# Kernel optimization log

Hardware: AMD Instinct MI355X
Metric: run time of the kernel (lower is better)

The kernel has to match this reference:

```python
import jax, jax.numpy as jnp
import numpy as np

N_NODES = 50000


def gcn_conv(x, src, dst, W, b, n):
    # PyG GCNConv: h = x @ W; add self-loops; sym-norm aggregate; + bias
    h = x @ W
    loop = jnp.arange(n, dtype=src.dtype)
    s = jnp.concatenate([src, loop])
    d = jnp.concatenate([dst, loop])
    deg = jax.ops.segment_sum(jnp.ones(s.shape[0], h.dtype), d, num_segments=n)
    dinv = jnp.where(deg > 0, jax.lax.rsqrt(deg), 0.0)
    norm = dinv[s] * dinv[d]  # [E+n]
    msg = h[s] * norm[:, None]  # [E+n, C] gather
    out = jax.ops.segment_sum(msg, d, num_segments=n)  # scatter-add
    return out + b


def mlp_decode(z, src, dst, Wa, ba, Wb, bb):
    feat = jnp.concatenate([z[src], z[dst]], axis=1)  # [P, 2*out]
    hid = jax.nn.relu(feat @ Wa + ba)
    return hid @ Wb + bb  # [P, 1]


def setup_inputs() -> dict:
    key = jax.random.key(0)
    ks = jax.random.split(key, 12)
    in_c, hid_c, out_c = 128, 128, 64
    E, P = 800000, 200000
    x = jax.random.normal(ks[0], (N_NODES, in_c), dtype=jnp.float32)
    edge_index = jax.random.randint(ks[1], (2, E), 0, N_NODES, dtype=jnp.int64)
    pos_edge_index = jax.random.randint(ks[2], (2, P), 0, N_NODES, dtype=jnp.int64)
    neg_edge_index = jax.random.randint(ks[3], (2, P), 0, N_NODES, dtype=jnp.int64)
    s1 = 1.0 / np.sqrt(in_c)
    s2 = 1.0 / np.sqrt(hid_c)
    s3 = 1.0 / np.sqrt(2 * out_c)
    W1 = jax.random.uniform(ks[4], (in_c, hid_c), jnp.float32, -s1, s1)
    b1 = jnp.zeros((hid_c,), jnp.float32)
    W2 = jax.random.uniform(ks[5], (hid_c, out_c), jnp.float32, -s2, s2)
    b2 = jnp.zeros((out_c,), jnp.float32)
    Wa = jax.random.uniform(ks[6], (2 * out_c, hid_c), jnp.float32, -s3, s3)
    ba = jax.random.uniform(ks[7], (hid_c,), jnp.float32, -s3, s3)
    Wb = jax.random.uniform(ks[8], (hid_c, 1), jnp.float32, -s2, s2)
    bb = jax.random.uniform(ks[9], (1,), jnp.float32, -s2, s2)
    return {"x": x, "edge_index": edge_index, "pos_edge_index": pos_edge_index,
            "neg_edge_index": neg_edge_index, "W1": W1, "b1": b1, "W2": W2,
            "b2": b2, "Wa": Wa, "ba": ba, "Wb": Wb, "bb": bb}


def reference(x, edge_index, pos_edge_index, neg_edge_index,
              W1, b1, W2, b2, Wa, ba, Wb, bb):
    src, dst = edge_index[0], edge_index[1]
    n = x.shape[0]
    z = gcn_conv(x, src, dst, W1, b1, n)
    z = jax.nn.relu(z)  # dropout disabled in eval mode
    z = gcn_conv(z, src, dst, W2, b2, n)
    pos_pred = mlp_decode(z, pos_edge_index[0], pos_edge_index[1], Wa, ba, Wb, bb)
    neg_pred = mlp_decode(z, neg_edge_index[0], neg_edge_index[1], Wa, ba, Wb, bb)
    return (pos_pred, neg_pred)
```

## Files before the change

### kernel.cpp

```cpp
#include <hip/hip_runtime.h>
#include <hip/hip_bf16.h>
#include <hip/hip_fp16.h>

#define NODES 50000
#define NEDGE 800000
#define NPRED 200000

typedef __attribute__((ext_vector_type(8))) short bf16x8;
typedef __attribute__((ext_vector_type(8))) unsigned short u16x8;
typedef __attribute__((ext_vector_type(4))) float f32x4;

__device__ inline float bf2f(unsigned short u) {
    union { unsigned int i; float f; } v; v.i = ((unsigned int)u) << 16; return v.f;
}
__device__ inline unsigned short f2bf(float f) {
    __hip_bfloat16 b = __float2bfloat16(f);
    return *(unsigned short*)&b;
}

__global__ __launch_bounds__(256) void rank_count4(const int* __restrict__ dstv, int* __restrict__ cnt,
                                                   int* __restrict__ rank, int E4) {
    int i = blockIdx.x * 256 + threadIdx.x;
    if (i < E4) {
        int4 d4 = ((const int4*)dstv)[i];
        int4 r4;
        r4.x = atomicAdd(&cnt[d4.x], 1);
        r4.y = atomicAdd(&cnt[d4.y], 1);
        r4.z = atomicAdd(&cnt[d4.z], 1);
        r4.w = atomicAdd(&cnt[d4.w], 1);
        ((int4*)rank)[i] = r4;
    }
}

__global__ __launch_bounds__(256) void scan_bsum(const int* __restrict__ cnt, int* __restrict__ bsum, int n) {
    __shared__ int s[256];
    int t = threadIdx.x, b = blockIdx.x;
    int base = b * 1024 + t * 4;
    int sum = 0;
#pragma unroll
    for (int j = 0; j < 4; ++j) { int i = base + j; if (i < n) sum += cnt[i]; }
    s[t] = sum; __syncthreads();
    for (int off = 128; off >= 1; off >>= 1) {
        if (t < off) s[t] += s[t + off];
        __syncthreads();
    }
    if (t == 0) bsum[b] = s[0];
}

__global__ void scan_boff(const int* __restrict__ bsum, int* __restrict__ boff, int nb,
                          int* __restrict__ row_ptr, int n) {
    int t = threadIdx.x;
    int v = (t < nb) ? bsum[t] : 0;
    int orig = v;
    for (int off = 1; off < 64; off <<= 1) {
        int u = __shfl_up(v, off, 64);
        if (t >= off) v += u;
    }
    boff[t] = v - orig;
    if (t == 63) row_ptr[n] = v;
}

__global__ __launch_bounds__(256) void scan_write(const int* __restrict__ cnt, const int* __restrict__ boff,
                                                  int* __restrict__ row_ptr, float* __restrict__ dinv, int n) {
    __shared__ int s[256];
    int t = threadIdx.x, b = blockIdx.x;
    int base = b * 1024 + t * 4;
    int v[4]; int sum = 0;
#pragma unroll
    for (int j = 0; j < 4; ++j) { int i = base + j; v[j] = (i < n) ? cnt[i] : 0; sum += v[j]; }
    s[t] = sum; __syncthreads();
    for (int off = 1; off < 256; off <<= 1) {
        int u = (t >= off) ? s[t - off] : 0;
        __syncthreads();
        s[t] += u;
        __syncthreads();
    }
    int run = s[t] - sum + boff[b];
#pragma unroll
    for (int j = 0; j < 4; ++j) {
        int i = base + j;
        if (i < n) {
            row_ptr[i] = run; run += v[j];
            dinv[i] = rsqrtf((float)(v[j] + 1));
        }
    }
}

__global__ __launch_bounds__(256) void csr_fill2(const int* __restrict__ ei, const int* __restrict__ rank,
                                                 const int* __restrict__ row_ptr, int* __restrict__ colv, int E4) {
    int i = blockIdx.x * 256 + threadIdx.x;
    if (i < E4) {
        int4 s4 = ((const int4*)ei)[i];
        int4 d4 = ((const int4*)(ei + NEDGE))[i];
        int4 r4 = ((const int4*)rank)[i];
        colv[row_ptr[d4.x] + r4.x] = s4.x;
        colv[row_ptr[d4.y] + r4.y] = s4.y;
        colv[row_ptr[d4.z] + r4.z] = s4.z;
        colv[row_ptr[d4.w] + r4.w] = s4.w;
    }
}

__global__ __launch_bounds__(256) void perm_all(const float* __restrict__ W1, const float* __restrict__ W2,
                                                const float* __restrict__ Wa,
                                                unsigned short* __restrict__ pW1,
                                                unsigned short* __restrict__ pW2,
                                                unsigned short* __restrict__ pWa) {
    int t = blockIdx.x * 256 + threadIdx.x;
    if (t >= 5120) return;
    const float* W; unsigned short* P; int N;
    if (t < 2048)      { W = W1; P = pW1; N = 128; }
    else if (t < 3072) { W = W2; P = pW2; N = 64;  t -= 2048; }
    else               { W = Wa; P = pWa; N = 128; t -= 3072; }
    int lane = t & 63;
    int kt = (t >> 6) & 3;
    int nt = t >> 8;
    int n = nt * 16 + (lane & 15);
    int k0 = kt * 32 + (lane >> 4) * 8;
#pragma unroll
    for (int j = 0; j < 8; ++j) P[t * 8 + j] = f2bf(W[(k0 + j) * N + n]);
}

template <int NT, bool AFP32>
__global__ __launch_bounds__(256) void gemm_mfma(const void* __restrict__ Xv,
                                                 const unsigned short* __restrict__ perm,
                                                 unsigned short* __restrict__ H, int M) {
    int w = blockIdx.x * 4 + (threadIdx.x >> 6);
    int m0 = w * 16;
    if (m0 >= M) return;
    int lane = threadIdx.x & 63;
    int m = lane & 15, q = lane >> 4;
    size_t row = (size_t)(m0 + m);
    bf16x8 a[4];
    if (AFP32) {
        const float* X = (const float*)Xv;
#pragma unroll
        for (int kt = 0; kt < 4; ++kt) {
            float4 f0 = *(const float4*)&X[row * 128 + kt * 32 + q * 8];
            float4 f1 = *(const float4*)&X[row * 128 + kt * 32 + q * 8 + 4];
            bf16x8 av;
            av[0] = (short)f2bf(f0.x); av[1] = (short)f2bf(f0.y);
            av[2] = (short)f2bf(f0.z); av[3] = (short)f2bf(f0.w);
            av[4] = (short)f2bf(f1.x); av[5] = (short)f2bf(f1.y);
            av[6] = (short)f2bf(f1.z); av[7] = (short)f2bf(f1.w);
            a[kt] = av;
        }
    } else {
        const unsigned short* X = (const unsigned short*)Xv;
#pragma unroll
        for (int kt = 0; kt < 4; ++kt)
            a[kt] = *(const bf16x8*)&X[row * 128 + kt * 32 + q * 8];
    }
    const int N = NT * 16;
#pragma unroll
    for (int nt = 0; nt < NT; ++nt) {
        f32x4 c = {0.f, 0.f, 0.f, 0.f};
#pragma unroll
        for (int kt = 0; kt < 4; ++kt) {
            bf16x8 b = *(const bf16x8*)(perm + (size_t)((nt * 4 + kt) * 64 + lane) * 8);
            c = __builtin_amdgcn_mfma_f32_16x16x32_bf16(a[kt], b, c, 0, 0, 0);
        }
#pragma unroll
        for (int r = 0; r < 4; ++r)
            H[(size_t)(m0 + q * 4 + r) * N + nt * 16 + m] = f2bf(c[r]);
    }
}

template <int C, bool RELU>
__global__ __launch_bounds__(256) void agg_bf16(const unsigned short* __restrict__ h,
                                                const int* __restrict__ row_ptr, const int* __restrict__ colv,
                                                const float* __restrict__ dinv, const float* __restrict__ bias,
                                                unsigned short* __restrict__ out) {
    constexpr int TPN = C / 8;
    constexpr int NPB = 256 / TPN;
    int d = blockIdx.x * NPB + threadIdx.x / TPN;
    if (d >= NODES) return;
    int c8 = (threadIdx.x % TPN) * 8;
    float dv = dinv[d];
    float acc[8];
    u16x8 self = *(const u16x8*)&h[(size_t)d * C + c8];
#pragma unroll
    for (int j = 0; j < 8; ++j) acc[j] = bf2f(self[j]) * dv;
    int i = row_ptr[d], end = row_ptr[d + 1];
    for (; i + 3 < end; i += 4) {
        int s0 = colv[i], s1 = colv[i + 1], s2 = colv[i + 2], s3 = colv[i + 3];
        float w0 = dinv[s0], w1 = dinv[s1], w2 = dinv[s2], w3 = dinv[s3];
        u16x8 r0 = *(const u16x8*)&h[(size_t)s0 * C + c8];
        u16x8 r1 = *(const u16x8*)&h[(size_t)s1 * C + c8];
        u16x8 r2 = *(const u16x8*)&h[(size_t)s2 * C + c8];
        u16x8 r3 = *(const u16x8*)&h[(size_t)s3 * C + c8];
#pragma unroll
        for (int j = 0; j < 8; ++j)
            acc[j] += bf2f(r0[j]) * w0 + bf2f(r1[j]) * w1 + bf2f(r2[j]) * w2 + bf2f(r3[j]) * w3;
    }
    for (; i < end; ++i) {
        int s0 = colv[i];
        float w0 = dinv[s0];
        u16x8 r0 = *(const u16x8*)&h[(size_t)s0 * C + c8];
#pragma unroll
        for (int j = 0; j < 8; ++j) acc[j] += bf2f(r0[j]) * w0;
    }
    u16x8 ov;
#pragma unroll
    for (int j = 0; j < 8; ++j) {
        float o = acc[j] * dv + bias[c8 + j];
        if (RELU) o = fmaxf(o, 0.f);
        ov[j] = f2bf(o);
    }
    *(u16x8*)&out[(size_t)d * C + c8] = ov;
}

__global__ __launch_bounds__(256) void decode_mfma2(const unsigned short* __restrict__ zb,
                                                    const int* __restrict__ pos, const int* __restrict__ neg,
                                                    const unsigned short* __restrict__ perm,
                                                    const float* __restrict__ ba, const float* __restrict__ Wb,
                                                    const float* __restrict__ bb, float* __restrict__ out, int P) {
    int lane = threadIdx.x & 63;
    int w = blockIdx.x * 4 + (threadIdx.x >> 6);
    int g0 = w * 4;
    if (g0 >= 12500) return;
    int m = lane & 15, q = lane >> 4;
    float bav[8], wbv[8];
#pragma unroll
    for (int nt = 0; nt < 8; ++nt) { bav[nt] = ba[nt * 16 + m]; wbv[nt] = Wb[nt * 16 + m]; }
    float bbv = bb[0];

    int idxS[3][2], idxD[3][2], base[3];
    bf16x8 A[2][8];

    auto loadIdx = [&](int it) {
        int slot = it % 3;
        int g = g0 + it;
        int half = (g >= 6250) ? 1 : 0;
        const int* src = half ? neg : pos;
        int e0 = (g - half * 6250) * 32;
        base[slot] = half * P + e0;
        int eA = e0 + m, eB = e0 + 16 + m;
        idxS[slot][0] = src[eA]; idxD[slot][0] = src[P + eA];
        idxS[slot][1] = src[eB]; idxD[slot][1] = src[P + eB];
    };
    auto loadFrags = [&](int it) {
        int slot = it % 3, buf = it & 1;
        size_t s0 = (size_t)idxS[slot][0] * 64, d0 = (size_t)idxD[slot][0] * 64;
        size_t s1 = (size_t)idxS[slot][1] * 64, d1 = (size_t)idxD[slot][1] * 64;
        A[buf][0] = *(const bf16x8*)(zb + s0 + q * 8);
        A[buf][1] = *(const bf16x8*)(zb + s0 + 32 + q * 8);
        A[buf][2] = *(const bf16x8*)(zb + d0 + q * 8);
        A[buf][3] = *(const bf16x8*)(zb + d0 + 32 + q * 8);
        A[buf][4] = *(const bf16x8*)(zb + s1 + q * 8);
        A[buf][5] = *(const bf16x8*)(zb + s1 + 32 + q * 8);
        A[buf][6] = *(const bf16x8*)(zb + d1 + q * 8);
        A[buf][7] = *(const bf16x8*)(zb + d1 + 32 + q * 8);
    };

    loadIdx(0); loadIdx(1); loadFrags(0);
#pragma unroll
    for (int it = 0; it < 4; ++it) {
        if (it + 2 < 4) loadIdx(it + 2);
        if (it + 1 < 4) loadFrags(it + 1);
        int buf = it & 1;
        float p0[4] = {0.f, 0.f, 0.f, 0.f};
        float p1[4] = {0.f, 0.f, 0.f, 0.f};
#pragma unroll
        for (int nt = 0; nt < 8; ++nt) {
            f32x4 c0 = {0.f, 0.f, 0.f, 0.f};
            f32x4 c1 = {0.f, 0.f, 0.f, 0.f};
#pragma unroll
            for (int kt = 0; kt < 4; ++kt) {
                bf16x8 b = *(const bf16x8*)(perm + (size_t)((nt * 4 + kt) * 64 + lane) * 8);
                c0 = __builtin_amdgcn_mfma_f32_16x16x32_bf16(A[buf][kt], b, c0, 0, 0, 0);
                c1 = __builtin_amdgcn_mfma_f32_16x16x32_bf16(A[buf][4 + kt], b, c1, 0, 0, 0);
            }
#pragma unroll
            for (int r = 0; r < 4; ++r) {
                p0[r] += fmaxf(c0[r] + bav[nt], 0.f) * wbv[nt];
                p1[r] += fmaxf(c1[r] + bav[nt], 0.f) * wbv[nt];
            }
        }
#pragma unroll
        for (int off = 1; off <= 8; off <<= 1) {
#pragma unroll
            for (int r = 0; r < 4; ++r) {
                p0[r] += __shfl_xor(p0[r], off, 64);
                p1[r] += __shfl_xor(p1[r], off, 64);
            }
        }
        if (m == 0) {
            int slot = it % 3;
            float4 st0 = { p0[0] + bbv, p0[1] + bbv, p0[2] + bbv, p0[3] + bbv };
            float4 st1 = { p1[0] + bbv, p1[1] + bbv, p1[2] + bbv, p1[3] + bbv };
            *(float4*)&out[base[slot] + q * 4] = st0;
            *(float4*)&out[base[slot] + 16 + q * 4] = st1;
        }
    }
}

extern "C" void kernel_launch(void* const* d_in, const int* in_sizes, int n_in,
                              void* d_out, int out_size, void* d_ws, size_t ws_size,
                              hipStream_t stream) {
    const int N = NODES, E = NEDGE, P = NPRED;
    const float* x  = (const float*)d_in[0];
    const int*   ei = (const int*)d_in[1];
    const int*  pos = (const int*)d_in[2];
    const int*  neg = (const int*)d_in[3];
    const float* W1 = (const float*)d_in[4];
    const float* b1 = (const float*)d_in[5];
    const float* W2 = (const float*)d_in[6];
    const float* b2 = (const float*)d_in[7];
    const float* Wa = (const float*)d_in[8];
    const float* ba = (const float*)d_in[9];
    const float* Wb = (const float*)d_in[10];
    const float* bb = (const float*)d_in[11];
    float* out = (float*)d_out;

    char* w = (char*)d_ws;
    auto alloc = [&](size_t bytes) { char* p = w; w += (bytes + 255) & ~(size_t)255; return p; };
    int*   cnt     = (int*)alloc((size_t)N * 4);
    int*   rankb   = (int*)alloc((size_t)E * 4);
    int*   row_ptr = (int*)alloc((size_t)(N + 1) * 4);
    int*   colv    = (int*)alloc((size_t)E * 4);
    float* dinv    = (float*)alloc((size_t)N * 4);
    int*   bsum    = (int*)alloc(64 * 4);
    int*   boff    = (int*)alloc(64 * 4);
    unsigned short* h1b = (unsigned short*)alloc((size_t)N * 128 * 2);
    unsigned short* z1b = (unsigned short*)alloc((size_t)N * 128 * 2);
    unsigned short* h2b = (unsigned short*)alloc((size_t)N * 64 * 2);
    unsigned short* zb  = (unsigned short*)alloc((size_t)N * 64 * 2);
    unsigned short* pW1 = (unsigned short*)alloc(2048 * 8 * 2);
    unsigned short* pW2 = (unsigned short*)alloc(1024 * 8 * 2);
    unsigned short* pWa = (unsigned short*)alloc(2048 * 8 * 2);

    const int nb = (N + 1023) / 1024;
    hipMemsetAsync(cnt, 0, (size_t)N * 4, stream);
    rank_count4<<<(E / 4 + 255) / 256, 256, 0, stream>>>(ei + E, cnt, rankb, E / 4);
    scan_bsum<<<nb, 256, 0, stream>>>(cnt, bsum, N);
    scan_boff<<<1, 64, 0, stream>>>(bsum, boff, nb, row_ptr, N);
    scan_write<<<nb, 256, 0, stream>>>(cnt, boff, row_ptr, dinv, N);
    csr_fill2<<<(E / 4 + 255) / 256, 256, 0, stream>>>(ei, rankb, row_ptr, colv, E / 4);

    perm_all<<<20, 256, 0, stream>>>(W1, W2, Wa, pW1, pW2, pWa);

    gemm_mfma<8, true><<<782, 256, 0, stream>>>(x, pW1, h1b, N);
    agg_bf16<128, true><<<N / 16, 256, 0, stream>>>(h1b, row_ptr, colv, dinv, b1, z1b);

    gemm_mfma<4, false><<<782, 256, 0, stream>>>(z1b, pW2, h2b, N);
    agg_bf16<64, false><<<(N + 31) / 32, 256, 0, stream>>>(h2b, row_ptr, colv, dinv, b2, zb);

    decode_mfma2<<<782, 256, 0, stream>>>(zb, pos, neg, pWa, ba, Wb, bb, out, P);
}
```

Before: 260.6 us.

## Degree-sort nodes for aggregation, unroll gathers by 8, stage decode weights in LDS

Fuses the weight permutation into the rank-count kernel, removing one launch. Builds a degree histogram and a node order sorted by in-degree so that aggregation wavefronts handle nodes of similar degree, reducing divergence. Widens the aggregation gather loop to 8 outstanding loads per iteration. In the decoder, copies the permuted Wa into shared memory and splits the MFMA accumulation into two independent chains. This adds two small kernels and extra index indirection, and gives up the natural write locality of the unsorted node order.

After: 248.5 us. 1.05x faster.

```diff
diff --git a/kernel.cpp b/kernel.cpp
--- a/kernel.cpp
+++ b/kernel.cpp
@@ -18,18 +18,40 @@
     return *(unsigned short*)&b;
 }
 
-__global__ __launch_bounds__(256) void rank_count4(const int* __restrict__ dstv, int* __restrict__ cnt,
-                                                   int* __restrict__ rank, int E4) {
-    int i = blockIdx.x * 256 + threadIdx.x;
-    if (i < E4) {
-        int4 d4 = ((const int4*)dstv)[i];
-        int4 r4;
-        r4.x = atomicAdd(&cnt[d4.x], 1);
-        r4.y = atomicAdd(&cnt[d4.y], 1);
-        r4.z = atomicAdd(&cnt[d4.z], 1);
-        r4.w = atomicAdd(&cnt[d4.w], 1);
-        ((int4*)rank)[i] = r4;
-    }
+#define RANK_BLOCKS 782
+__global__ __launch_bounds__(256) void rank_perm(const int* __restrict__ dstv, int* __restrict__ cnt,
+                                                 int* __restrict__ rank, int E4,
+                                                 const float* __restrict__ W1, const float* __restrict__ W2,
+                                                 const float* __restrict__ Wa,
+                                                 unsigned short* __restrict__ pW1,
+                                                 unsigned short* __restrict__ pW2,
+                                                 unsigned short* __restrict__ pWa) {
+    if (blockIdx.x < RANK_BLOCKS) {
+        int i = blockIdx.x * 256 + threadIdx.x;
+        if (i < E4) {
+            int4 d4 = ((const int4*)dstv)[i];
+            int4 r4;
+            r4.x = atomicAdd(&cnt[d4.x], 1);
+            r4.y = atomicAdd(&cnt[d4.y], 1);
+            r4.z = atomicAdd(&cnt[d4.z], 1);
+            r4.w = atomicAdd(&cnt[d4.w], 1);
+            ((int4*)rank)[i] = r4;
+        }
+        return;
+    }
+    int t = (blockIdx.x - RANK_BLOCKS) * 256 + threadIdx.x;
+    if (t >= 5120) return;
+    const float* W; unsigned short* P; int N;
+    if (t < 2048)      { W = W1; P = pW1; N = 128; }
+    else if (t < 3072) { W = W2; P = pW2; N = 64;  t -= 2048; }
+    else               { W = Wa; P = pWa; N = 128; t -= 3072; }
+    int lane = t & 63;
+    int kt = (t >> 6) & 3;
+    int nt = t >> 8;
+    int n = nt * 16 + (lane & 15);
+    int k0 = kt * 32 + (lane >> 4) * 8;
+#pragma unroll
+    for (int j = 0; j < 8; ++j) P[t * 8 + j] = f2bf(W[(k0 + j) * N + n]);
 }
 
 __global__ __launch_bounds__(256) void scan_bsum(const int* __restrict__ cnt, int* __restrict__ bsum, int n) {
@@ -61,9 +83,12 @@
 }
 
 __global__ __launch_bounds__(256) void scan_write(const int* __restrict__ cnt, const int* __restrict__ boff,
-                                                  int* __restrict__ row_ptr, float* __restrict__ dinv, int n) {
+                                                  int* __restrict__ row_ptr, float* __restrict__ dinv,
+                                                  int* __restrict__ hist, int* __restrict__ rank2, int n) {
     __shared__ int s[256];
+    __shared__ int lh[64], lbase[64];
     int t = threadIdx.x, b = blockIdx.x;
+    if (t < 64) lh[t] = 0;
     int base = b * 1024 + t * 4;
     int v[4]; int sum = 0;
 #pragma unroll
@@ -76,13 +101,44 @@
         __syncthreads();
     }
     int run = s[t] - sum + boff[b];
+    int lr[4], bin[4];
 #pragma unroll
     for (int j = 0; j < 4; ++j) {
         int i = base + j;
         if (i < n) {
             row_ptr[i] = run; run += v[j];
             dinv[i] = rsqrtf((float)(v[j] + 1));
-        }
+            bin[j] = v[j] < 63 ? v[j] : 63;
+            lr[j] = atomicAdd(&lh[bin[j]], 1);
+        }
+    }
+    __syncthreads();
+    if (t < 64) lbase[t] = atomicAdd(&hist[t], lh[t]);
+    __syncthreads();
+#pragma unroll
+    for (int j = 0; j < 4; ++j) {
+        int i = base + j;
+        if (i < n) rank2[i] = lbase[bin[j]] + lr[j];
+    }
+}
+
+__global__ void scan_hist(int* __restrict__ hist) {
+    int t = threadIdx.x;
+    int v = hist[t];
+    int orig = v;
+    for (int off = 1; off < 64; off <<= 1) {
+        int u = __shfl_up(v, off, 64);
+        if (t >= off) v += u;
+    }
+    hist[t] = v - orig;
+}
+
+__global__ __launch_bounds__(256) void scatter_order(const int* __restrict__ cnt, const int* __restrict__ rank2,
+                                                     const int* __restrict__ hist, int* __restrict__ order, int n) {
+    int i = blockIdx.x * 256 + threadIdx.x;
+    if (i < n) {
+        int d = cnt[i] < 63 ? cnt[i] : 63;
+        order[hist[d] + rank2[i]] = i;
     }
 }
 
@@ -98,26 +154,6 @@
         colv[row_ptr[d4.z] + r4.z] = s4.z;
         colv[row_ptr[d4.w] + r4.w] = s4.w;
     }
-}
-
-__global__ __launch_bounds__(256) void perm_all(const float* __restrict__ W1, const float* __restrict__ W2,
-                                                const float* __restrict__ Wa,
-                                                unsigned short* __restrict__ pW1,
-                                                unsigned short* __restrict__ pW2,
-                                                unsigned short* __restrict__ pWa) {
-    int t = blockIdx.x * 256 + threadIdx.x;
-    if (t >= 5120) return;
-    const float* W; unsigned short* P; int N;
-    if (t < 2048)      { W = W1; P = pW1; N = 128; }
-    else if (t < 3072) { W = W2; P = pW2; N = 64;  t -= 2048; }
-    else               { W = Wa; P = pWa; N = 128; t -= 3072; }
-    int lane = t & 63;
-    int kt = (t >> 6) & 3;
-    int nt = t >> 8;
-    int n = nt * 16 + (lane & 15);
-    int k0 = kt * 32 + (lane >> 4) * 8;
-#pragma unroll
-    for (int j = 0; j < 8; ++j) P[t * 8 + j] = f2bf(W[(k0 + j) * N + n]);
 }
 
 template <int NT, bool AFP32>
@@ -169,11 +205,13 @@
 __global__ __launch_bounds__(256) void agg_bf16(const unsigned short* __restrict__ h,
                                                 const int* __restrict__ row_ptr, const int* __restrict__ colv,
                                                 const float* __restrict__ dinv, const float* __restrict__ bias,
+                                                const int* __restrict__ order,
                                                 unsigned short* __restrict__ out) {
     constexpr int TPN = C / 8;
     constexpr int NPB = 256 / TPN;
-    int d = blockIdx.x * NPB + threadIdx.x / TPN;
-    if (d >= NODES) return;
+    int g = blockIdx.x * NPB + threadIdx.x / TPN;
+    if (g >= NODES) return;
+    int d = order[g];
     int c8 = (threadIdx.x % TPN) * 8;
     float dv = dinv[d];
     float acc[8];
@@ -181,16 +219,31 @@
 #pragma unroll
     for (int j = 0; j < 8; ++j) acc[j] = bf2f(self[j]) * dv;
     int i = row_ptr[d], end = row_ptr[d + 1];
+    for (; i + 7 < end; i += 8) {
+        int s[8]; float w[8]; u16x8 r[8];
+#pragma unroll
+        for (int k = 0; k < 8; ++k) s[k] = colv[i + k];
+#pragma unroll
+        for (int k = 0; k < 8; ++k) w[k] = dinv[s[k]];
+#pragma unroll
+        for (int k = 0; k < 8; ++k) r[k] = *(const u16x8*)&h[(size_t)s[k] * C + c8];
+#pragma unroll
+        for (int k = 0; k < 8; ++k)
+#pragma unroll
+            for (int j = 0; j < 8; ++j) acc[j] += bf2f(r[k][j]) * w[k];
+    }
     for (; i + 3 < end; i += 4) {
-        int s0 = colv[i], s1 = colv[i + 1], s2 = colv[i + 2], s3 = colv[i + 3];
-        float w0 = dinv[s0], w1 = dinv[s1], w2 = dinv[s2], w3 = dinv[s3];
-        u16x8 r0 = *(const u16x8*)&h[(size_t)s0 * C + c8];
-        u16x8 r1 = *(const u16x8*)&h[(size_t)s1 * C + c8];
-        u16x8 r2 = *(const u16x8*)&h[(size_t)s2 * C + c8];
-        u16x8 r3 = *(const u16x8*)&h[(size_t)s3 * C + c8];
-#pragma unroll
-        for (int j = 0; j < 8; ++j)
-            acc[j] += bf2f(r0[j]) * w0 + bf2f(r1[j]) * w1 + bf2f(r2[j]) * w2 + bf2f(r3[j]) * w3;
+        int s[4]; float w[4]; u16x8 r[4];
+#pragma unroll
+        for (int k = 0; k < 4; ++k) s[k] = colv[i + k];
+#pragma unroll
+        for (int k = 0; k < 4; ++k) w[k] = dinv[s[k]];
+#pragma unroll
+        for (int k = 0; k < 4; ++k) r[k] = *(const u16x8*)&h[(size_t)s[k] * C + c8];
+#pragma unroll
+        for (int k = 0; k < 4; ++k)
+#pragma unroll
+            for (int j = 0; j < 8; ++j) acc[j] += bf2f(r[k][j]) * w[k];
     }
     for (; i < end; ++i) {
         int s0 = colv[i];
@@ -209,24 +262,30 @@
     *(u16x8*)&out[(size_t)d * C + c8] = ov;
 }
 
-__global__ __launch_bounds__(256) void decode_mfma2(const unsigned short* __restrict__ zb,
+__global__ __launch_bounds__(256) void decode_mfma4(const unsigned short* __restrict__ zb,
                                                     const int* __restrict__ pos, const int* __restrict__ neg,
                                                     const unsigned short* __restrict__ perm,
                                                     const float* __restrict__ ba, const float* __restrict__ Wb,
                                                     const float* __restrict__ bb, float* __restrict__ out, int P) {
-    int lane = threadIdx.x & 63;
-    int w = blockIdx.x * 4 + (threadIdx.x >> 6);
-    int g0 = w * 4;
-    if (g0 >= 12500) return;
+    __shared__ unsigned short sB[2048 * 8];
+    int tid = threadIdx.x;
+#pragma unroll
+    for (int i = tid * 8; i < 2048 * 8; i += 256 * 8)
+        *(u16x8*)&sB[i] = *(const u16x8*)&perm[i];
+    __syncthreads();
+
+    int w = blockIdx.x * 4 + (tid >> 6);
+    if (w >= 3125) return;
+    int lane = tid & 63;
     int m = lane & 15, q = lane >> 4;
     float bav[8], wbv[8];
 #pragma unroll
     for (int nt = 0; nt < 8; ++nt) { bav[nt] = ba[nt * 16 + m]; wbv[nt] = Wb[nt * 16 + m]; }
     float bbv = bb[0];
+    int g0 = w * 4;
 
     int idxS[3][2], idxD[3][2], base[3];
     bf16x8 A[2][8];
-
     auto loadIdx = [&](int it) {
         int slot = it % 3;
         int g = g0 + it;
@@ -234,11 +293,10 @@
         const int* src = half ? neg : pos;
         int e0 = (g - half * 6250) * 32;
         base[slot] = half * P + e0;
-        int eA = e0 + m, eB = e0 + 16 + m;
-        idxS[slot][0] = src[eA]; idxD[slot][0] = src[P + eA];
-        idxS[slot][1] = src[eB]; idxD[slot][1] = src[P + eB];
+        idxS[slot][0] = src[e0 + m];      idxD[slot][0] = src[P + e0 + m];
+        idxS[slot][1] = src[e0 + 16 + m]; idxD[slot][1] = src[P + e0 + 16 + m];
     };
-    auto loadFrags = [&](int it) {
+    auto loadA = [&](int it) {
         int slot = it % 3, buf = it & 1;
         size_t s0 = (size_t)idxS[slot][0] * 64, d0 = (size_t)idxD[slot][0] * 64;
         size_t s1 = (size_t)idxS[slot][1] * 64, d1 = (size_t)idxD[slot][1] * 64;
@@ -252,28 +310,34 @@
         A[buf][7] = *(const bf16x8*)(zb + d1 + 32 + q * 8);
     };
 
-    loadIdx(0); loadIdx(1); loadFrags(0);
+    loadIdx(0); loadIdx(1); loadA(0);
 #pragma unroll
     for (int it = 0; it < 4; ++it) {
         if (it + 2 < 4) loadIdx(it + 2);
-        if (it + 1 < 4) loadFrags(it + 1);
+        if (it + 1 < 4) loadA(it + 1);
         int buf = it & 1;
         float p0[4] = {0.f, 0.f, 0.f, 0.f};
         float p1[4] = {0.f, 0.f, 0.f, 0.f};
 #pragma unroll
         for (int nt = 0; nt < 8; ++nt) {
-            f32x4 c0 = {0.f, 0.f, 0.f, 0.f};
-            f32x4 c1 = {0.f, 0.f, 0.f, 0.f};
-#pragma unroll
-            for (int kt = 0; kt < 4; ++kt) {
-                bf16x8 b = *(const bf16x8*)(perm + (size_t)((nt * 4 + kt) * 64 + lane) * 8);
-                c0 = __builtin_amdgcn_mfma_f32_16x16x32_bf16(A[buf][kt], b, c0, 0, 0, 0);
-                c1 = __builtin_amdgcn_mfma_f32_16x16x32_bf16(A[buf][4 + kt], b, c1, 0, 0, 0);
-            }
+            bf16x8 b0 = *(const bf16x8*)&sB[(size_t)((nt * 4 + 0) * 64 + lane) * 8];
+            bf16x8 b1 = *(const bf16x8*)&sB[(size_t)((nt * 4 + 1) * 64 + lane) * 8];
+            bf16x8 b2 = *(const bf16x8*)&sB[(size_t)((nt * 4 + 2) * 64 + lane) * 8];
+            bf16x8 b3 = *(const bf16x8*)&sB[(size_t)((nt * 4 + 3) * 64 + lane) * 8];
+            f32x4 c0a = {0.f, 0.f, 0.f, 0.f}, c0b = {0.f, 0.f, 0.f, 0.f};
+            f32x4 c1a = {0.f, 0.f, 0.f, 0.f}, c1b = {0.f, 0.f, 0.f, 0.f};
+            c0a = __builtin_amdgcn_mfma_f32_16x16x32_bf16(A[buf][0], b0, c0a, 0, 0, 0);
+            c1a = __builtin_amdgcn_mfma_f32_16x16x32_bf16(A[buf][4], b0, c1a, 0, 0, 0);
+            c0b = __builtin_amdgcn_mfma_f32_16x16x32_bf16(A[buf][2], b2, c0b, 0, 0, 0);
+            c1b = __builtin_amdgcn_mfma_f32_16x16x32_bf16(A[buf][6], b2, c1b, 0, 0, 0);
+            c0a = __builtin_amdgcn_mfma_f32_16x16x32_bf16(A[buf][1], b1, c0a, 0, 0, 0);
+            c1a = __builtin_amdgcn_mfma_f32_16x16x32_bf16(A[buf][5], b1, c1a, 0, 0, 0);
+            c0b = __builtin_amdgcn_mfma_f32_16x16x32_bf16(A[buf][3], b3, c0b, 0, 0, 0);
+            c1b = __builtin_amdgcn_mfma_f32_16x16x32_bf16(A[buf][7], b3, c1b, 0, 0, 0);
 #pragma unroll
             for (int r = 0; r < 4; ++r) {
-                p0[r] += fmaxf(c0[r] + bav[nt], 0.f) * wbv[nt];
-                p1[r] += fmaxf(c1[r] + bav[nt], 0.f) * wbv[nt];
+                p0[r] += fmaxf(c0a[r] + c0b[r] + bav[nt], 0.f) * wbv[nt];
+                p1[r] += fmaxf(c1a[r] + c1b[r] + bav[nt], 0.f) * wbv[nt];
             }
         }
 #pragma unroll
@@ -314,8 +378,11 @@
 
     char* w = (char*)d_ws;
     auto alloc = [&](size_t bytes) { char* p = w; w += (bytes + 255) & ~(size_t)255; return p; };
-    int*   cnt     = (int*)alloc((size_t)N * 4);
+    int*   cnt     = (int*)alloc((size_t)(N + 64) * 4);
+    int*   hist    = cnt + N;
     int*   rankb   = (int*)alloc((size_t)E * 4);
+    int*   rank2   = (int*)alloc((size_t)N * 4);
+    int*   order   = (int*)alloc((size_t)N * 4);
     int*   row_ptr = (int*)alloc((size_t)(N + 1) * 4);
     int*   colv    = (int*)alloc((size_t)E * 4);
     float* dinv    = (float*)alloc((size_t)N * 4);
@@ -330,20 +397,21 @@
     unsigned short* pWa = (unsigned short*)alloc(2048 * 8 * 2);
 
     const int nb = (N + 1023) / 1024;
-    hipMemsetAsync(cnt, 0, (size_t)N * 4, stream);
-    rank_count4<<<(E / 4 + 255) / 256, 256, 0, stream>>>(ei + E, cnt, rankb, E / 4);
+    hipMemsetAsync(cnt, 0, (size_t)(N + 64) * 4, stream);
+    rank_perm<<<RANK_BLOCKS + 20, 256, 0, stream>>>(ei + E, cnt, rankb, E / 4,
+                                                    W1, W2, Wa, pW1, pW2, pWa);
     scan_bsum<<<nb, 256, 0, stream>>>(cnt, bsum, N);
     scan_boff<<<1, 64, 0, stream>>>(bsum, boff, nb, row_ptr, N);
-    scan_write<<<nb, 256, 0, stream>>>(cnt, boff, row_ptr, dinv, N);
+    scan_write<<<nb, 256, 0, stream>>>(cnt, boff, row_ptr, dinv, hist, rank2, N);
+    scan_hist<<<1, 64, 0, stream>>>(hist);
+    scatter_order<<<(N + 255) / 256, 256, 0, stream>>>(cnt, rank2, hist, order, N);
     csr_fill2<<<(E / 4 + 255) / 256, 256, 0, stream>>>(ei, rankb, row_ptr, colv, E / 4);
 
-    perm_all<<<20, 256, 0, stream>>>(W1, W2, Wa, pW1, pW2, pWa);
-
     gemm_mfma<8, true><<<782, 256, 0, stream>>>(x, pW1, h1b, N);
-    agg_bf16<128, true><<<N / 16, 256, 0, stream>>>(h1b, row_ptr, colv, dinv, b1, z1b);
+    agg_bf16<128, true><<<N / 16, 256, 0, stream>>>(h1b, row_ptr, colv, dinv, b1, order, z1b);
 
     gemm_mfma<4, false><<<782, 256, 0, stream>>>(z1b, pW2, h2b, N);
-    agg_bf16<64, false><<<(N + 31) / 32, 256, 0, stream>>>(h2b, row_ptr, colv, dinv, b2, zb);
-
-    decode_mfma2<<<782, 256, 0, stream>>>(zb, pos, neg, pWa, ba, Wb, bb, out, P);
-}
+    agg_bf16<64, false><<<(N + 31) / 32, 256, 0, stream>>>(h2b, row_ptr, colv, dinv, b2, order, zb);
+
+    decode_mfma4<<<782, 256, 0, stream>>>(zb, pos, neg, pWa, ba, Wb, bb, out, P);
+}
```
